# Optimization experiments

Measured on AMD Instinct MI355X. Metric: run time of the kernel, lower is better.

Reference implementation:

```python
import jax, jax.numpy as jnp
import numpy as np

N_EMBED = 768
N_HEAD = 12
HEAD = N_EMBED // N_HEAD
B, T = 4, 2048


def setup_inputs() -> dict:
    key = jax.random.key(0)
    ks = jax.random.split(key, 12)
    s = 0.02
    d = N_EMBED
    return {
        "x": jax.random.normal(ks[0], (B, T, d), jnp.float32),
        "ln1_g": jnp.ones((d,), jnp.float32),
        "ln1_b": jnp.zeros((d,), jnp.float32),
        "w_attn": jax.random.normal(ks[1], (d, 3 * d), jnp.float32) * s,
        "b_attn": jnp.zeros((3 * d,), jnp.float32),
        "w_aproj": jax.random.normal(ks[2], (d, d), jnp.float32) * s,
        "b_aproj": jnp.zeros((d,), jnp.float32),
        "ln2_g": jnp.ones((d,), jnp.float32),
        "ln2_b": jnp.zeros((d,), jnp.float32),
        "w_fc": jax.random.normal(ks[3], (d, 4 * d), jnp.float32) * s,
        "b_fc": jnp.zeros((4 * d,), jnp.float32),
        "w_mproj": jax.random.normal(ks[4], (4 * d, d), jnp.float32) * s,
        "b_mproj": jnp.zeros((d,), jnp.float32),
    }


def _layernorm(x, g, b, eps=1e-5):
    mu = jnp.mean(x, axis=-1, keepdims=True)
    var = jnp.var(x, axis=-1, keepdims=True)
    return (x - mu) * jax.lax.rsqrt(var + eps) * g + b


def _attn(x, w_attn, b_attn, w_aproj, b_aproj):
    Bq, Tq, C = x.shape
    qkv = x @ w_attn + b_attn  # [B,T,3C]
    q, k, v = jnp.split(qkv, 3, axis=2)
    q = q.reshape(Bq, Tq, N_HEAD, HEAD).transpose(0, 2, 1, 3)  # [B,H,T,hd]
    k = k.reshape(Bq, Tq, N_HEAD, HEAD).transpose(0, 2, 1, 3)
    v = v.reshape(Bq, Tq, N_HEAD, HEAD).transpose(0, 2, 1, 3)
    att = jnp.einsum("bhqd,bhkd->bhqk", q, k) * (1.0 / np.sqrt(HEAD))
    causal = jnp.tril(jnp.ones((Tq, Tq), bool))
    att = jnp.where(causal, att, -jnp.inf)
    att = jax.nn.softmax(att, axis=-1)
    y = jnp.einsum("bhqk,bhkd->bhqd", att, v)
    y = y.transpose(0, 2, 1, 3).reshape(Bq, Tq, C)
    return y @ w_aproj + b_aproj


def reference(x, ln1_g, ln1_b, w_attn, b_attn, w_aproj, b_aproj,
              ln2_g, ln2_b, w_fc, b_fc, w_mproj, b_mproj):
    x = x + _attn(_layernorm(x, ln1_g, ln1_b), w_attn, b_attn, w_aproj, b_aproj)
    h = _layernorm(x, ln2_g, ln2_b)
    h = jax.nn.gelu(h @ w_fc + b_fc, approximate=False)
    x = x + (h @ w_mproj + b_mproj)
    return x
```

## Files before the change

### kernel.cpp

```cpp
#include <hip/hip_runtime.h>
#include <hip/hip_bf16.h>

#define NE 768
#define NH 12
#define HD 64
#define BB 4
#define TT 2048
#define ROWS (BB*TT)
#define QSCALE 0.18033688011112042f

typedef __attribute__((ext_vector_type(8))) short bf16x8;
typedef __attribute__((ext_vector_type(4))) float f32x4;

#define WAITV(N) asm volatile("s_waitcnt vmcnt(" #N ")" ::: "memory")
#define BARSYNC()                                   \
  do {                                              \
    __builtin_amdgcn_sched_barrier(0);              \
    __builtin_amdgcn_s_barrier();                   \
    __builtin_amdgcn_sched_barrier(0);              \
  } while (0)

__device__ __forceinline__ short f2bf(float f) {
  __hip_bfloat16 h = __float2bfloat16(f);
  union { __hip_bfloat16 h; short s; } u; u.h = h; return u.s;
}

__device__ __forceinline__ float exp2fast(float x) {
  float r;
  asm("v_exp_f32 %0, %1" : "=v"(r) : "v"(x));
  return r;
}

__device__ __forceinline__ float rcpfast(float x) {
  float r;
  asm("v_rcp_f32 %0, %1" : "=v"(r) : "v"(x));
  return r;
}

__device__ __forceinline__ unsigned int cvtpk(float lo, float hi) {
  unsigned int r;
  asm("v_cvt_pk_bf16_f32 %0, %1, %2" : "=v"(r) : "v"(lo), "v"(hi));
  return r;
}

__device__ __forceinline__ float gelu_fast(float v) {
  float u = fmaf(0.044715f * v, v, 1.0f);
  float e = exp2fast(fminf(v * u * 2.3022079f, 80.f));
  return v * e * rcpfast(e + 1.f);
}

__device__ __forceinline__ void gload16(const void* g, void* l) {
  __builtin_amdgcn_global_load_lds(
      (const __attribute__((address_space(1))) void*)g,
      (__attribute__((address_space(3))) void*)l,
      16, 0, 0);
}

__device__ __forceinline__ void xcd_remap(int id, int nbn, int& bm, int& bn) {
  int x = id & 7;
  int j = id >> 3;
  bm = x * 8 + j / nbn;
  bn = j % nbn;
}

__global__ __launch_bounds__(256) void wtrans_all_kernel(
    const float* __restrict__ w_attn, const float* __restrict__ w_aproj,
    const float* __restrict__ w_fc, const float* __restrict__ w_mproj,
    short* __restrict__ o_attn, short* __restrict__ o_aproj,
    short* __restrict__ o_fc, short* __restrict__ o_mproj) {
  __shared__ short tile[64 * 65];
  int id = blockIdx.x;
  const float* W; short* Wt; int K, N, bx, by;
  if (id < 432)       { W = w_attn;  Wt = o_attn;  K = 768;  N = 2304; bx = id % 12;  by = id / 12; }
  else if (id < 576)  { id -= 432;  W = w_aproj; Wt = o_aproj; K = 768;  N = 768;  bx = id % 12;  by = id / 12; }
  else if (id < 1152) { id -= 576;  W = w_fc;    Wt = o_fc;    K = 768;  N = 3072; bx = id % 12;  by = id / 12; }
  else                { id -= 1152; W = w_mproj; Wt = o_mproj; K = 3072; N = 768;  bx = id % 48;  by = id / 48; }
  int k0 = bx * 64, n0 = by * 64;
  int t = threadIdx.x;
#pragma unroll
  for (int p = 0; p < 16; ++p) {
    int idx = p * 256 + t;
    int r = idx >> 6, c = idx & 63;
    tile[r * 65 + c] = f2bf(W[(size_t)(k0 + r) * N + n0 + c]);
  }
  __syncthreads();
#pragma unroll
  for (int p = 0; p < 16; ++p) {
    int idx = p * 256 + t;
    int rr = idx >> 6, cc = idx & 63;
    Wt[(size_t)(n0 + rr) * K + k0 + cc] = tile[cc * 65 + rr];
  }
}

__global__ __launch_bounds__(256) void vtrans_kernel(
    const short* __restrict__ qkv, short* __restrict__ vt) {
  __shared__ short tile[64 * 65];
  int bh = blockIdx.x;
  int b = bh / NH, h = bh % NH;
  int t0 = blockIdx.y * 64;
  int t = threadIdx.x;
#pragma unroll
  for (int p = 0; p < 16; ++p) {
    int idx = p * 256 + t;
    int r = idx >> 6, c = idx & 63;
    tile[r * 65 + c] =
        qkv[(size_t)(b * TT + t0 + r) * (3 * NE) + 2 * NE + h * HD + c];
  }
  __syncthreads();
#pragma unroll
  for (int p = 0; p < 16; ++p) {
    int idx = p * 256 + t;
    int rr = idx >> 6, cc = idx & 63;
    vt[(size_t)bh * HD * TT + (size_t)rr * TT + t0 + cc] = tile[cc * 65 + rr];
  }
}

__global__ __launch_bounds__(64) void ln_kernel(
    const float* __restrict__ x, const float* __restrict__ g,
    const float* __restrict__ b, short* __restrict__ out) {
  int row = blockIdx.x, l = threadIdx.x;
  const float* xr = x + (size_t)row * NE;
  float4 v[3];
  float s = 0.f, ss = 0.f;
#pragma unroll
  for (int i = 0; i < 3; ++i) {
    v[i] = *reinterpret_cast<const float4*>(xr + l * 4 + i * 256);
    s += v[i].x + v[i].y + v[i].z + v[i].w;
    ss += v[i].x * v[i].x + v[i].y * v[i].y + v[i].z * v[i].z + v[i].w * v[i].w;
  }
#pragma unroll
  for (int m = 1; m < 64; m <<= 1) {
    s += __shfl_xor(s, m);
    ss += __shfl_xor(ss, m);
  }
  float mu = s * (1.0f / NE);
  float var = ss * (1.0f / NE) - mu * mu;
  float rstd = rsqrtf(var + 1e-5f);
#pragma unroll
  for (int i = 0; i < 3; ++i) {
    float4 gv = *reinterpret_cast<const float4*>(g + l * 4 + i * 256);
    float4 bv = *reinterpret_cast<const float4*>(b + l * 4 + i * 256);
    short4 o;
    o.x = f2bf((v[i].x - mu) * rstd * gv.x + bv.x);
    o.y = f2bf((v[i].y - mu) * rstd * gv.y + bv.y);
    o.z = f2bf((v[i].z - mu) * rstd * gv.z + bv.z);
    o.w = f2bf((v[i].w - mu) * rstd * gv.w + bv.w);
    *reinterpret_cast<short4*>(out + (size_t)row * NE + l * 4 + i * 256) = o;
  }
}


template <int EPI>
__global__ __launch_bounds__(256) void gemm_kernel(
    const short* __restrict__ A, const short* __restrict__ Bt,
    const float* __restrict__ bias, const float* __restrict__ resid,
    void* __restrict__ Cout, int M, int N, int K, int nbn) {
  __shared__ short As[3][128 * 32];
  __shared__ short Bs[3][128 * 32];
  int t = threadIdx.x;
  int w = t >> 6, l = t & 63;
  int wr = w >> 1, wc = w & 1;
  int bm, bn;
  xcd_remap(blockIdx.x, nbn, bm, bn);
  int lr = l & 15, g4 = l >> 4;

  f32x4 acc[4][4];
#pragma unroll
  for (int i = 0; i < 4; ++i)
#pragma unroll
    for (int j = 0; j < 4; ++j) acc[i][j] = (f32x4){0.f, 0.f, 0.f, 0.f};

  int r0 = t >> 2;
  int cs = ((t & 3) ^ (r0 & 3) ^ ((r0 >> 2) & 3)) * 8;
  const short* ga = A + (size_t)(bm * 128) * K;
  const short* gb = Bt + (size_t)(bn * 128) * K;

#pragma unroll
  for (int p = 0; p < 2; ++p) {
    int ko = p * 32;
    gload16(ga + (size_t)r0 * K + ko + cs, &As[p][t * 8]);
    gload16(ga + (size_t)(r0 + 64) * K + ko + cs, &As[p][(t + 256) * 8]);
    gload16(gb + (size_t)r0 * K + ko + cs, &Bs[p][t * 8]);
    gload16(gb + (size_t)(r0 + 64) * K + ko + cs, &Bs[p][(t + 256) * 8]);
  }

  int xorR = ((lr & 3) ^ ((lr >> 2) & 3)) << 4;
  int nk = K >> 5;
  int cur = 0, prv = 2;
  for (int kt = 0; kt < nk; ++kt) {
    if (kt < nk - 1) WAITV(4); else WAITV(0);
    BARSYNC();
    if (kt + 2 < nk) {
      int ko = (kt + 2) * 32;
      gload16(ga + (size_t)r0 * K + ko + cs, &As[prv][t * 8]);
      gload16(ga + (size_t)(r0 + 64) * K + ko + cs, &As[prv][(t + 256) * 8]);
      gload16(gb + (size_t)r0 * K + ko + cs, &Bs[prv][t * 8]);
      gload16(gb + (size_t)(r0 + 64) * K + ko + cs, &Bs[prv][(t + 256) * 8]);
    }
    __builtin_amdgcn_sched_barrier(0);
    const char* Ab = (const char*)As[cur];
    const char* Bb = (const char*)Bs[cur];
    bf16x8 af[4], bfr[4];
#pragma unroll
    for (int i = 0; i < 4; ++i)
      af[i] = *reinterpret_cast<const bf16x8*>(
          Ab + (((wr * 64 + i * 16 + lr) * 64 + g4 * 16) ^ xorR));
#pragma unroll
    for (int j = 0; j < 4; ++j)
      bfr[j] = *reinterpret_cast<const bf16x8*>(
          Bb + (((wc * 64 + j * 16 + lr) * 64 + g4 * 16) ^ xorR));
#pragma unroll
    for (int i = 0; i < 4; ++i)
#pragma unroll
      for (int j = 0; j < 4; ++j)
        acc[i][j] = __builtin_amdgcn_mfma_f32_16x16x32_bf16(af[i], bfr[j], acc[i][j], 0, 0, 0);
    prv = cur;
    cur = (cur == 2) ? 0 : cur + 1;
  }

  int rbase = bm * 128 + wr * 64;
  int cbase = bn * 128 + wc * 64;
#pragma unroll
  for (int i = 0; i < 4; ++i) {
#pragma unroll
    for (int r = 0; r < 4; ++r) {
      int row = rbase + i * 16 + g4 * 4 + r;
#pragma unroll
      for (int j = 0; j < 4; ++j) {
        int col = cbase + j * 16 + lr;
        float v = acc[i][j][r] + bias[col];
        if (EPI == 0) {
          if (col < NE) v *= QSCALE;
          ((short*)Cout)[(size_t)row * N + col] = f2bf(v);
        } else if (EPI == 1) {
          ((short*)Cout)[(size_t)row * N + col] = f2bf(gelu_fast(v));
        } else {
          ((float*)Cout)[(size_t)row * N + col] = v + resid[(size_t)row * N + col];
        }
      }
    }
  }
}

template <int EPI>
__global__ __launch_bounds__(256) void gemm64_kernel(
    const short* __restrict__ A, const short* __restrict__ Bt,
    const float* __restrict__ bias, const float* __restrict__ resid,
    void* __restrict__ Cout, int M, int N, int K, int nbn) {
  __shared__ short As[4][128 * 32];
  __shared__ short Bs[4][64 * 32];
  int t = threadIdx.x;
  int w = t >> 6, l = t & 63;
  int bm, bn;
  xcd_remap(blockIdx.x, nbn, bm, bn);
  int lr = l & 15, g4 = l >> 4;

  f32x4 acc[2][4];
#pragma unroll
  for (int i = 0; i < 2; ++i)
#pragma unroll
    for (int j = 0; j < 4; ++j) acc[i][j] = (f32x4){0.f, 0.f, 0.f, 0.f};

  int r0 = t >> 2;
  int cs = ((t & 3) ^ (r0 & 3) ^ ((r0 >> 2) & 3)) * 8;
  const short* ga = A + (size_t)(bm * 128) * K;
  const short* gb = Bt + (size_t)(bn * 64) * K;

#pragma unroll
  for (int p = 0; p < 3; ++p) {
    int ko = p * 32;
    gload16(ga + (size_t)r0 * K + ko + cs, &As[p][t * 8]);
    gload16(ga + (size_t)(r0 + 64) * K + ko + cs, &As[p][(t + 256) * 8]);
    gload16(gb + (size_t)r0 * K + ko + cs, &Bs[p][t * 8]);
  }

  int xorR = ((lr & 3) ^ ((lr >> 2) & 3)) << 4;
  int nk = K >> 5;
  for (int kt = 0; kt < nk; ++kt) {
    int bi = kt & 3;
    int rem = nk - 1 - kt;
    if (rem >= 2) WAITV(6);
    else if (rem == 1) WAITV(3);
    else WAITV(0);
    BARSYNC();
    if (kt + 3 < nk) {
      int ko = (kt + 3) * 32;
      int nb = (kt + 3) & 3;
      gload16(ga + (size_t)r0 * K + ko + cs, &As[nb][t * 8]);
      gload16(ga + (size_t)(r0 + 64) * K + ko + cs, &As[nb][(t + 256) * 8]);
      gload16(gb + (size_t)r0 * K + ko + cs, &Bs[nb][t * 8]);
    }
    __builtin_amdgcn_sched_barrier(0);
    const char* Ab = (const char*)As[bi];
    const char* Bb = (const char*)Bs[bi];
    bf16x8 af[2], bfr[4];
#pragma unroll
    for (int i = 0; i < 2; ++i)
      af[i] = *reinterpret_cast<const bf16x8*>(
          Ab + (((w * 32 + i * 16 + lr) * 64 + g4 * 16) ^ xorR));
#pragma unroll
    for (int j = 0; j < 4; ++j)
      bfr[j] = *reinterpret_cast<const bf16x8*>(
          Bb + (((j * 16 + lr) * 64 + g4 * 16) ^ xorR));
#pragma unroll
    for (int i = 0; i < 2; ++i)
#pragma unroll
      for (int j = 0; j < 4; ++j)
        acc[i][j] = __builtin_amdgcn_mfma_f32_16x16x32_bf16(af[i], bfr[j], acc[i][j], 0, 0, 0);
  }

  int rbase = bm * 128 + w * 32;
  int cbase = bn * 64;
#pragma unroll
  for (int i = 0; i < 2; ++i) {
#pragma unroll
    for (int r = 0; r < 4; ++r) {
      int row = rbase + i * 16 + g4 * 4 + r;
#pragma unroll
      for (int j = 0; j < 4; ++j) {
        int col = cbase + j * 16 + lr;
        float v = acc[i][j][r] + bias[col];
        if (EPI == 0) {
          ((short*)Cout)[(size_t)row * N + col] = f2bf(v);
        } else if (EPI == 1) {
          ((short*)Cout)[(size_t)row * N + col] = f2bf(gelu_fast(v));
        } else {
          ((float*)Cout)[(size_t)row * N + col] = v + resid[(size_t)row * N + col];
        }
      }
    }
  }
}

__global__ __launch_bounds__(256, 4) void attn_kernel(
    const short* __restrict__ qkv, const short* __restrict__ vt,
    short* __restrict__ y) {
  __shared__ short Ks[2][64 * 64];
  __shared__ short Vs[2][64 * 64];
  int t = threadIdx.x, w = t >> 6, l = t & 63;
  int lr = l & 15, g = l >> 4, lkb = g * 8;
  int bh = blockIdx.x;
  int b = bh / NH, h = bh % NH;
  int qt = ((int)gridDim.y - 1) - blockIdx.y;
  int qbase = qt * 64;
  const int rstride = 3 * NE;

  const short* qrow = qkv + (size_t)(b * TT + qbase + w * 16 + lr) * rstride + h * HD + lkb;
  bf16x8 qf0 = *reinterpret_cast<const bf16x8*>(qrow);
  bf16x8 qf1 = *reinterpret_cast<const bf16x8*>(qrow + 32);

  f32x4 o[4];
#pragma unroll
  for (int j = 0; j < 4; ++j) o[j] = (f32x4){0.f, 0.f, 0.f, 0.f};
  float m_run = -3e38f, l_run = 0.f;

  int ci0 = t, ci1 = t + 256;
  int row0 = ci0 >> 3, c0 = ((ci0 & 7) ^ (row0 & 7)) * 8;
  int row1 = ci1 >> 3, c1 = ((ci1 & 7) ^ (row1 & 7)) * 8;

  const short* kbase = qkv + (size_t)(b * TT) * rstride + NE + h * HD;
  const short* vtb = vt + (size_t)bh * HD * TT;

  gload16(kbase + (size_t)row0 * rstride + c0, &Ks[0][ci0 * 8]);
  gload16(kbase + (size_t)row1 * rstride + c1, &Ks[0][ci1 * 8]);
  gload16(vtb + (size_t)row0 * TT + c0, &Vs[0][ci0 * 8]);
  gload16(vtb + (size_t)row1 * TT + c1, &Vs[0][ci1 * 8]);

  int qmin = qbase + w * 16;
  int srcA = ((g & 1) * 2) * 16 + lr;
  int srcB = srcA + 16;
  bool ghi = (g >= 2);

  int nkv = qt + 1;
  for (int kt = 0; kt < nkv; ++kt) {
    int bi = kt & 1;
    int kvbase = kt * 64;
    bool pre = (kt + 1 < nkv);
    __syncthreads();

    if (pre) {
      int nb = kvbase + 64;
      gload16(kbase + (size_t)(nb + row0) * rstride + c0, &Ks[bi ^ 1][ci0 * 8]);
      gload16(kbase + (size_t)(nb + row1) * rstride + c1, &Ks[bi ^ 1][ci1 * 8]);
      gload16(vtb + (size_t)row0 * TT + nb + c0, &Vs[bi ^ 1][ci0 * 8]);
      gload16(vtb + (size_t)row1 * TT + nb + c1, &Vs[bi ^ 1][ci1 * 8]);
    }

    f32x4 s[4];
#pragma unroll
    for (int nt = 0; nt < 4; ++nt) {
      int row = nt * 16 + lr;
      bf16x8 kf0 = *reinterpret_cast<const bf16x8*>(
          (char*)Ks[bi] + ((row * 128 + lkb * 2) ^ ((lr & 7) << 4)));
      bf16x8 kf1 = *reinterpret_cast<const bf16x8*>(
          (char*)Ks[bi] + ((row * 128 + 64 + lkb * 2) ^ ((lr & 7) << 4)));
      f32x4 st = (f32x4){0.f, 0.f, 0.f, 0.f};
      st = __builtin_amdgcn_mfma_f32_16x16x32_bf16(kf0, qf0, st, 0, 0, 0);
      st = __builtin_amdgcn_mfma_f32_16x16x32_bf16(kf1, qf1, st, 0, 0, 0);
      s[nt] = st;
    }

    if (kvbase + 63 > qmin) {
      int qabs = qmin + lr;
#pragma unroll
      for (int nt = 0; nt < 4; ++nt)
#pragma unroll
        for (int r = 0; r < 4; ++r) {
          int kp = kvbase + nt * 16 + g * 4 + r;
          s[nt][r] = (kp <= qabs) ? s[nt][r] : -3e38f;
        }
    }

    float mx = s[0][0];
#pragma unroll
    for (int nt = 0; nt < 4; ++nt)
#pragma unroll
      for (int r = 0; r < 4; ++r) mx = fmaxf(mx, s[nt][r]);
    mx = fmaxf(mx, __shfl_xor(mx, 16));
    mx = fmaxf(mx, __shfl_xor(mx, 32));
    if (__any(mx > m_run + 11.54f)) {
      float mn = fmaxf(m_run, mx);
      float al = exp2fast(m_run - mn);
      m_run = mn;
      l_run *= al;
      float al0 = __shfl(al, g * 4 + 0);
      float al1 = __shfl(al, g * 4 + 1);
      float al2 = __shfl(al, g * 4 + 2);
      float al3 = __shfl(al, g * 4 + 3);
#pragma unroll
      for (int j = 0; j < 4; ++j) {
        o[j][0] *= al0; o[j][1] *= al1; o[j][2] *= al2; o[j][3] *= al3;
      }
    }
    float rs = 0.f;
#pragma unroll
    for (int nt = 0; nt < 4; ++nt)
#pragma unroll
      for (int r = 0; r < 4; ++r) {
        float p = exp2fast(s[nt][r] - m_run);
        s[nt][r] = p;
        rs += p;
      }
    rs += __shfl_xor(rs, 16);
    rs += __shfl_xor(rs, 32);
    l_run += rs;

    unsigned int pw[4][2];
#pragma unroll
    for (int nt = 0; nt < 4; ++nt)
#pragma unroll
      for (int pr = 0; pr < 2; ++pr)
        pw[nt][pr] = cvtpk(s[nt][2 * pr], s[nt][2 * pr + 1]);

#pragma unroll
    for (int c = 0; c < 2; ++c) {
      unsigned int a00 = __shfl(pw[c * 2 + 0][0], srcA);
      unsigned int a01 = __shfl(pw[c * 2 + 0][1], srcA);
      unsigned int a02 = __shfl(pw[c * 2 + 0][0], srcB);
      unsigned int a03 = __shfl(pw[c * 2 + 0][1], srcB);
      unsigned int a10 = __shfl(pw[c * 2 + 1][0], srcA);
      unsigned int a11 = __shfl(pw[c * 2 + 1][1], srcA);
      unsigned int a12 = __shfl(pw[c * 2 + 1][0], srcB);
      unsigned int a13 = __shfl(pw[c * 2 + 1][1], srcB);
      union { unsigned int u[4]; bf16x8 v; } pau;
      pau.u[0] = ghi ? a10 : a00;
      pau.u[1] = ghi ? a11 : a01;
      pau.u[2] = ghi ? a12 : a02;
      pau.u[3] = ghi ? a13 : a03;
#pragma unroll
      for (int j = 0; j < 4; ++j) {
        int vrow = j * 16 + lr;
        bf16x8 vf = *reinterpret_cast<const bf16x8*>(
            (char*)Vs[bi] + ((vrow * 128 + c * 64 + lkb * 2) ^ ((lr & 7) << 4)));
        o[j] = __builtin_amdgcn_mfma_f32_16x16x32_bf16(pau.v, vf, o[j], 0, 0, 0);
      }
    }
  }

  float inv = 1.0f / l_run;
  float i0 = __shfl(inv, g * 4 + 0);
  float i1 = __shfl(inv, g * 4 + 1);
  float i2 = __shfl(inv, g * 4 + 2);
  float i3 = __shfl(inv, g * 4 + 3);
#pragma unroll
  for (int r = 0; r < 4; ++r) {
    float ir = (r == 0) ? i0 : (r == 1) ? i1 : (r == 2) ? i2 : i3;
    size_t row = (size_t)(b * TT + qbase + w * 16 + g * 4 + r);
#pragma unroll
    for (int j = 0; j < 4; ++j)
      y[row * NE + h * HD + j * 16 + lr] = f2bf(o[j][r] * ir);
  }
}

extern "C" void kernel_launch(void* const* d_in, const int* in_sizes, int n_in,
                              void* d_out, int out_size, void* d_ws, size_t ws_size,
                              hipStream_t stream) {
  (void)in_sizes; (void)n_in; (void)out_size; (void)ws_size;
  const float* x       = (const float*)d_in[0];
  const float* ln1_g   = (const float*)d_in[1];
  const float* ln1_b   = (const float*)d_in[2];
  const float* w_attn  = (const float*)d_in[3];
  const float* b_attn  = (const float*)d_in[4];
  const float* w_aproj = (const float*)d_in[5];
  const float* b_aproj = (const float*)d_in[6];
  const float* ln2_g   = (const float*)d_in[7];
  const float* ln2_b   = (const float*)d_in[8];
  const float* w_fc    = (const float*)d_in[9];
  const float* b_fc    = (const float*)d_in[10];
  const float* w_mproj = (const float*)d_in[11];
  const float* b_mproj = (const float*)d_in[12];

  char* ws = (char*)d_ws;
  size_t off = 0;
  auto alloc = [&](size_t bytes) {
    char* p = ws + off;
    off += (bytes + 255) & ~(size_t)255;
    return p;
  };
  short* wt_attn  = (short*)alloc((size_t)2304 * 768 * 2);
  short* wt_aproj = (short*)alloc((size_t)768 * 768 * 2);
  short* wt_fc    = (short*)alloc((size_t)3072 * 768 * 2);
  short* wt_mproj = (short*)alloc((size_t)768 * 3072 * 2);
  short* lnb  = (short*)alloc((size_t)ROWS * 768 * 2);
  short* qkvb = (short*)alloc((size_t)ROWS * 3072 * 2);
  short* yb   = (short*)alloc((size_t)ROWS * 768 * 2);
  float* x2   = (float*)alloc((size_t)ROWS * 768 * 4);
  short* vtg = lnb;

  wtrans_all_kernel<<<1728, 256, 0, stream>>>(
      w_attn, w_aproj, w_fc, w_mproj, wt_attn, wt_aproj, wt_fc, wt_mproj);

  ln_kernel<<<ROWS, 64, 0, stream>>>(x, ln1_g, ln1_b, lnb);
  gemm_kernel<0><<<64 * 18, 256, 0, stream>>>(
      lnb, wt_attn, b_attn, nullptr, qkvb, ROWS, 2304, 768, 18);
  vtrans_kernel<<<dim3(BB * NH, TT / 64), 256, 0, stream>>>(qkvb, vtg);
  attn_kernel<<<dim3(BB * NH, TT / 64), 256, 0, stream>>>(qkvb, vtg, yb);
  gemm64_kernel<2><<<64 * 12, 256, 0, stream>>>(
      yb, wt_aproj, b_aproj, x, x2, ROWS, 768, 768, 12);
  ln_kernel<<<ROWS, 64, 0, stream>>>(x2, ln2_g, ln2_b, lnb);
  gemm_kernel<1><<<64 * 24, 256, 0, stream>>>(
      lnb, wt_fc, b_fc, nullptr, qkvb, ROWS, 3072, 768, 24);
  gemm64_kernel<2><<<64 * 12, 256, 0, stream>>>(
      qkvb, wt_mproj, b_mproj, x2, (float*)d_out, ROWS, 768, 3072, 12);
}
```

Before: 283.0 us.

## Replace 128x64 GEMM with 128x256 tiles and simplify LDS swizzle

Adds a 128x256-tile GEMM kernel, used for the QKV and FC projections, in which each wave computes a 64x128 sub-tile. The attention-projection and MLP-projection GEMMs move from the 128x64 kernel to the 128x128 kernel. The LDS XOR swizzle drops its second term, keeping only the low two row bits. Larger tiles aim to raise arithmetic intensity and cut global re-reads, but they halve or quarter the block count, to 384 blocks for the N=768 GEMMs. They also raise register pressure and risk LDS bank conflicts under the weaker swizzle.

```diff
diff --git a/kernel.cpp b/kernel.cpp
--- a/kernel.cpp
+++ b/kernel.cpp
@@ -149,7 +149,6 @@
   }
 }
 
-
 template <int EPI>
 __global__ __launch_bounds__(256) void gemm_kernel(
     const short* __restrict__ A, const short* __restrict__ Bt,
@@ -171,7 +170,7 @@
     for (int j = 0; j < 4; ++j) acc[i][j] = (f32x4){0.f, 0.f, 0.f, 0.f};
 
   int r0 = t >> 2;
-  int cs = ((t & 3) ^ (r0 & 3) ^ ((r0 >> 2) & 3)) * 8;
+  int cs = ((t & 3) ^ (r0 & 3)) * 8;
   const short* ga = A + (size_t)(bm * 128) * K;
   const short* gb = Bt + (size_t)(bn * 128) * K;
 
@@ -184,7 +183,7 @@
     gload16(gb + (size_t)(r0 + 64) * K + ko + cs, &Bs[p][(t + 256) * 8]);
   }
 
-  int xorR = ((lr & 3) ^ ((lr >> 2) & 3)) << 4;
+  int xorR = (lr & 3) << 4;
   int nk = K >> 5;
   int cur = 0, prv = 2;
   for (int kt = 0; kt < nk; ++kt) {
@@ -243,84 +242,90 @@
 }
 
 template <int EPI>
-__global__ __launch_bounds__(256) void gemm64_kernel(
+__global__ __launch_bounds__(256, 2) void gemm256_kernel(
     const short* __restrict__ A, const short* __restrict__ Bt,
     const float* __restrict__ bias, const float* __restrict__ resid,
     void* __restrict__ Cout, int M, int N, int K, int nbn) {
-  __shared__ short As[4][128 * 32];
-  __shared__ short Bs[4][64 * 32];
+  __shared__ short As[3][128 * 32];
+  __shared__ short Bs[3][256 * 32];
   int t = threadIdx.x;
   int w = t >> 6, l = t & 63;
+  int wr = w >> 1, wc = w & 1;
   int bm, bn;
   xcd_remap(blockIdx.x, nbn, bm, bn);
   int lr = l & 15, g4 = l >> 4;
 
-  f32x4 acc[2][4];
-#pragma unroll
-  for (int i = 0; i < 2; ++i)
-#pragma unroll
-    for (int j = 0; j < 4; ++j) acc[i][j] = (f32x4){0.f, 0.f, 0.f, 0.f};
+  f32x4 acc[4][8];
+#pragma unroll
+  for (int i = 0; i < 4; ++i)
+#pragma unroll
+    for (int j = 0; j < 8; ++j) acc[i][j] = (f32x4){0.f, 0.f, 0.f, 0.f};
 
   int r0 = t >> 2;
-  int cs = ((t & 3) ^ (r0 & 3) ^ ((r0 >> 2) & 3)) * 8;
+  int cs = ((t & 3) ^ (r0 & 3)) * 8;
   const short* ga = A + (size_t)(bm * 128) * K;
-  const short* gb = Bt + (size_t)(bn * 64) * K;
-
-#pragma unroll
-  for (int p = 0; p < 3; ++p) {
+  const short* gb = Bt + (size_t)(bn * 256) * K;
+
+#pragma unroll
+  for (int p = 0; p < 2; ++p) {
     int ko = p * 32;
     gload16(ga + (size_t)r0 * K + ko + cs, &As[p][t * 8]);
     gload16(ga + (size_t)(r0 + 64) * K + ko + cs, &As[p][(t + 256) * 8]);
     gload16(gb + (size_t)r0 * K + ko + cs, &Bs[p][t * 8]);
-  }
-
-  int xorR = ((lr & 3) ^ ((lr >> 2) & 3)) << 4;
+    gload16(gb + (size_t)(r0 + 64) * K + ko + cs, &Bs[p][(t + 256) * 8]);
+    gload16(gb + (size_t)(r0 + 128) * K + ko + cs, &Bs[p][(t + 512) * 8]);
+    gload16(gb + (size_t)(r0 + 192) * K + ko + cs, &Bs[p][(t + 768) * 8]);
+  }
+
+  int xorR = (lr & 3) << 4;
   int nk = K >> 5;
+  int cur = 0, prv = 2;
   for (int kt = 0; kt < nk; ++kt) {
-    int bi = kt & 3;
-    int rem = nk - 1 - kt;
-    if (rem >= 2) WAITV(6);
-    else if (rem == 1) WAITV(3);
-    else WAITV(0);
+    if (kt < nk - 1) WAITV(6); else WAITV(0);
     BARSYNC();
-    if (kt + 3 < nk) {
-      int ko = (kt + 3) * 32;
-      int nb = (kt + 3) & 3;
-      gload16(ga + (size_t)r0 * K + ko + cs, &As[nb][t * 8]);
-      gload16(ga + (size_t)(r0 + 64) * K + ko + cs, &As[nb][(t + 256) * 8]);
-      gload16(gb + (size_t)r0 * K + ko + cs, &Bs[nb][t * 8]);
+    if (kt + 2 < nk) {
+      int ko = (kt + 2) * 32;
+      gload16(ga + (size_t)r0 * K + ko + cs, &As[prv][t * 8]);
+      gload16(ga + (size_t)(r0 + 64) * K + ko + cs, &As[prv][(t + 256) * 8]);
+      gload16(gb + (size_t)r0 * K + ko + cs, &Bs[prv][t * 8]);
+      gload16(gb + (size_t)(r0 + 64) * K + ko + cs, &Bs[prv][(t + 256) * 8]);
+      gload16(gb + (size_t)(r0 + 128) * K + ko + cs, &Bs[prv][(t + 512) * 8]);
+      gload16(gb + (size_t)(r0 + 192) * K + ko + cs, &Bs[prv][(t + 768) * 8]);
     }
     __builtin_amdgcn_sched_barrier(0);
-    const char* Ab = (const char*)As[bi];
-    const char* Bb = (const char*)Bs[bi];
-    bf16x8 af[2], bfr[4];
-#pragma unroll
-    for (int i = 0; i < 2; ++i)
+    const char* Ab = (const char*)As[cur];
+    const char* Bb = (const char*)Bs[cur];
+    bf16x8 af[4], bfr[8];
+#pragma unroll
+    for (int i = 0; i < 4; ++i)
       af[i] = *reinterpret_cast<const bf16x8*>(
-          Ab + (((w * 32 + i * 16 + lr) * 64 + g4 * 16) ^ xorR));
-#pragma unroll
-    for (int j = 0; j < 4; ++j)
+          Ab + (((wr * 64 + i * 16 + lr) * 64 + g4 * 16) ^ xorR));
+#pragma unroll
+    for (int j = 0; j < 8; ++j)
       bfr[j] = *reinterpret_cast<const bf16x8*>(
-          Bb + (((j * 16 + lr) * 64 + g4 * 16) ^ xorR));
-#pragma unroll
-    for (int i = 0; i < 2; ++i)
-#pragma unroll
-      for (int j = 0; j < 4; ++j)
+          Bb + (((wc * 128 + j * 16 + lr) * 64 + g4 * 16) ^ xorR));
+#pragma unroll
+    for (int i = 0; i < 4; ++i)
+#pragma unroll
+      for (int j = 0; j < 8; ++j)
         acc[i][j] = __builtin_amdgcn_mfma_f32_16x16x32_bf16(af[i], bfr[j], acc[i][j], 0, 0, 0);
-  }
-
-  int rbase = bm * 128 + w * 32;
-  int cbase = bn * 64;
-#pragma unroll
-  for (int i = 0; i < 2; ++i) {
+    prv = cur;
+    cur = (cur == 2) ? 0 : cur + 1;
+  }
+
+  int rbase = bm * 128 + wr * 64;
+  int cbase = bn * 256 + wc * 128;
+#pragma unroll
+  for (int i = 0; i < 4; ++i) {
 #pragma unroll
     for (int r = 0; r < 4; ++r) {
       int row = rbase + i * 16 + g4 * 4 + r;
 #pragma unroll
-      for (int j = 0; j < 4; ++j) {
+      for (int j = 0; j < 8; ++j) {
         int col = cbase + j * 16 + lr;
         float v = acc[i][j][r] + bias[col];
         if (EPI == 0) {
+          if (col < NE) v *= QSCALE;
           ((short*)Cout)[(size_t)row * N + col] = f2bf(v);
         } else if (EPI == 1) {
           ((short*)Cout)[(size_t)row * N + col] = f2bf(gelu_fast(v));
@@ -531,15 +536,15 @@
       w_attn, w_aproj, w_fc, w_mproj, wt_attn, wt_aproj, wt_fc, wt_mproj);
 
   ln_kernel<<<ROWS, 64, 0, stream>>>(x, ln1_g, ln1_b, lnb);
-  gemm_kernel<0><<<64 * 18, 256, 0, stream>>>(
-      lnb, wt_attn, b_attn, nullptr, qkvb, ROWS, 2304, 768, 18);
+  gemm256_kernel<0><<<64 * 9, 256, 0, stream>>>(
+      lnb, wt_attn, b_attn, nullptr, qkvb, ROWS, 2304, 768, 9);
   vtrans_kernel<<<dim3(BB * NH, TT / 64), 256, 0, stream>>>(qkvb, vtg);
   attn_kernel<<<dim3(BB * NH, TT / 64), 256, 0, stream>>>(qkvb, vtg, yb);
-  gemm64_kernel<2><<<64 * 12, 256, 0, stream>>>(
-      yb, wt_aproj, b_aproj, x, x2, ROWS, 768, 768, 12);
+  gemm_kernel<2><<<64 * 6, 256, 0, stream>>>(
+      yb, wt_aproj, b_aproj, x, x2, ROWS, 768, 768, 6);
   ln_kernel<<<ROWS, 64, 0, stream>>>(x2, ln2_g, ln2_b, lnb);
-  gemm_kernel<1><<<64 * 24, 256, 0, stream>>>(
-      lnb, wt_fc, b_fc, nullptr, qkvb, ROWS, 3072, 768, 24);
-  gemm64_kernel<2><<<64 * 12, 256, 0, stream>>>(
-      qkvb, wt_mproj, b_mproj, x2, (float*)d_out, ROWS, 768, 3072, 12);
-}
+  gemm256_kernel<1><<<64 * 12, 256, 0, stream>>>(
+      lnb, wt_fc, b_fc, nullptr, qkvb, ROWS, 3072, 768, 12);
+  gemm_kernel<2><<<64 * 6, 256, 0, stream>>>(
+      qkvb, wt_mproj, b_mproj, x2, (float*)d_out, ROWS, 768, 3072, 6);
+}
```

Measured after the change: 299.7 us. 1.06x slower.
